# Kernel optimization log

Measured on AMD Instinct MI355X. Metric: run time of the kernel, lower is better.

Reference implementation:

```python
import jax, jax.numpy as jnp
import numpy as np

TAU = 0.1
HARD_K = 32
MIN_OVERLAP = 4
PAIR_WEIGHTS = [("view", "cart", 0.2), ("cart", "purchase", 1.0), ("view", "purchase", 1.0)]


def setup_inputs() -> dict:
    key = jax.random.key(0)
    ks = jax.random.split(key, 6)
    U, D = 100000, 128
    return {
        "emb_view": jax.random.normal(ks[0], (U, D), dtype=jnp.float32),
        "emb_cart": jax.random.normal(ks[1], (U, D), dtype=jnp.float32),
        "emb_purchase": jax.random.normal(ks[2], (U, D), dtype=jnp.float32),
        "users_view": jax.random.randint(ks[3], (20000,), 0, U, dtype=jnp.int64),
        "users_cart": jax.random.randint(ks[4], (15000,), 0, U, dtype=jnp.int64),
        "users_purchase": jax.random.randint(ks[5], (10000,), 0, U, dtype=jnp.int64),
    }


def _l2norm(x):
    # F.normalize(x, dim=-1): x / max(||x||, eps)
    n = jnp.linalg.norm(x, axis=-1, keepdims=True)
    return x / jnp.maximum(n, 1e-12)


def _directional(z_weak, z_strong, tau, hard_k):
    N = z_strong.shape[0]
    if N < 2:
        return jnp.zeros((), dtype=z_strong.dtype)
    z_w = _l2norm(jax.lax.stop_gradient(z_weak))  # weak side is detached
    z_s = _l2norm(z_strong)
    sim = (z_s @ z_w.T) / tau  # [N, N]
    pos = jnp.diagonal(sim)    # positive logits, labels = arange(N)
    n_hard = min(hard_k, N - 1)
    if 0 < n_hard < N - 1:
        neg_only = jnp.where(jnp.eye(N, dtype=bool), -jnp.inf, sim)
        hard_neg, _ = jax.lax.top_k(neg_only, n_hard)          # [N, n_hard]
        logits = jnp.concatenate([pos[:, None], hard_neg], 1)  # [N, 1+n_hard]
        return jnp.mean(jax.scipy.special.logsumexp(logits, axis=1) - pos)
    # full-softmax CE with label i for row i
    return jnp.mean(jax.scipy.special.logsumexp(sim, axis=1) - pos)


def reference(emb_view, emb_cart, emb_purchase, users_view, users_cart, users_purchase):
    embs = {"view": emb_view, "cart": emb_cart, "purchase": emb_purchase}
    users = {
        "view": np.asarray(users_view),
        "cart": np.asarray(users_cart),
        "purchase": np.asarray(users_purchase),
    }
    loss = jnp.zeros((), dtype=emb_view.dtype)
    for weak, strong, w in PAIR_WEIGHTS:
        u_w, u_s = users[weak], users[strong]
        if u_w.size == 0 or u_s.size == 0:
            continue
        # common_pair = u_w[isin(u_w, u_s)] : keeps u_w order and duplicates
        common = u_w[np.isin(u_w, u_s)]
        if common.size < MIN_OVERLAP:
            continue
        idx = jnp.asarray(common)
        loss = loss + w * _directional(embs[weak][idx], embs[strong][idx], TAU, HARD_K)
    return loss
```

## Files before the change

kernel.cpp:

```cpp
#include <hip/hip_runtime.h>
#include <hip/hip_bf16.h>
#include <math.h>

#define D 128
#define NEG_INF (-3.0e38f)
#define LDA 136

#define C0 3200
#define C1 1792
#define C2 2304
#define T0 25
#define T1 14
#define T2 18

typedef __attribute__((ext_vector_type(8))) short bf16x8;
typedef __attribute__((ext_vector_type(8))) unsigned short u16x8;
typedef __attribute__((ext_vector_type(4))) float f32x4;

__device__ __forceinline__ float wredf_add(float v) {
#pragma unroll
  for (int m = 32; m; m >>= 1) v += __shfl_xor(v, m, 64);
  return v;
}
__device__ __forceinline__ float wredf_max(float v) {
#pragma unroll
  for (int m = 32; m; m >>= 1) v = fmaxf(v, __shfl_xor(v, m, 64));
  return v;
}
__device__ __forceinline__ float wredf_min(float v) {
#pragma unroll
  for (int m = 32; m; m >>= 1) v = fminf(v, __shfl_xor(v, m, 64));
  return v;
}
__device__ __forceinline__ int wredi_add(int v) {
#pragma unroll
  for (int m = 32; m; m >>= 1) v += __shfl_xor(v, m, 64);
  return v;
}

__global__ void build_masks_k(const int* __restrict__ uc, int nc,
                              const int* __restrict__ up, int npu,
                              unsigned* __restrict__ mc, unsigned* __restrict__ mp) {
  int t = blockIdx.x * blockDim.x + threadIdx.x;
  if (t < nc) {
    int u = uc[t];
    atomicOr(&mc[u >> 5], 1u << (u & 31));
  } else {
    int t2 = t - nc;
    if (t2 < npu) {
      int u = up[t2];
      atomicOr(&mp[u >> 5], 1u << (u & 31));
    }
  }
}

__global__ void filter_k(const int* __restrict__ uv, int nv,
                         const int* __restrict__ uc, int nc,
                         const unsigned* __restrict__ mc, const unsigned* __restrict__ mp,
                         int* __restrict__ c0, int* __restrict__ c1, int* __restrict__ c2,
                         int* __restrict__ counts, int s1, int s2) {
  int t = blockIdx.x * blockDim.x + threadIdx.x;
  int lane = threadIdx.x & 63;
  const int* src;
  const unsigned* m;
  int* dst;
  int* cnt;
  int n, cap, base;
  if (t < s1) {
    src = uv; n = nv; m = mc; dst = c0; cnt = counts + 0; cap = C0; base = t;
  } else if (t < s2) {
    src = uc; n = nc; m = mp; dst = c1; cnt = counts + 1; cap = C1; base = t - s1;
  } else {
    src = uv; n = nv; m = mp; dst = c2; cnt = counts + 2; cap = C2; base = t - s2;
  }
  bool match = false;
  int u = 0;
  if (base < n) {
    u = src[base];
    match = (m[u >> 5] >> (u & 31)) & 1u;
  }
  unsigned long long b = __ballot(match);
  int tot = __popcll(b);
  int idx0 = 0;
  if (lane == 0 && tot) idx0 = atomicAdd(cnt, tot);
  idx0 = __shfl(idx0, 0, 64);
  if (match) {
    int p = idx0 + __popcll(b & ((1ull << lane) - 1));
    if (p < cap) dst[p] = u;
  }
}

struct GatherArgs {
  const float* emb[6];
  const int* com[6];
  const int* cnt[6];
  short* dst[6];
  int start[7];
};

__global__ __launch_bounds__(256) void gather_norm_k(GatherArgs ga) {
  int wid = threadIdx.x >> 6, lane = threadIdx.x & 63;
  int g = blockIdx.x * 4 + wid;
  if (g >= ga.start[6]) return;
  int s = 0;
#pragma unroll
  for (int t = 1; t < 6; ++t)
    if (g >= ga.start[t]) s = t;
  int r = g - ga.start[s];
  int cap = ga.start[s + 1] - ga.start[s];
  int N = min(*ga.cnt[s], cap);
  short* drow = ga.dst[s] + (size_t)r * D + lane * 2;
  if (r >= N) {
    *(ushort2*)drow = make_ushort2(0, 0);
    return;
  }
  int u = ga.com[s][r];
  const float* src = ga.emb[s] + (size_t)u * D;
  float2 v = *(const float2*)(src + lane * 2);
  float ss = v.x * v.x + v.y * v.y;
  ss = wredf_add(ss);
  float inv = 1.0f / fmaxf(sqrtf(ss), 1e-12f);
  __hip_bfloat16 h0 = __float2bfloat16(v.x * inv);
  __hip_bfloat16 h1 = __float2bfloat16(v.y * inv);
  ushort2 o;
  o.x = *(unsigned short*)&h0;
  o.y = *(unsigned short*)&h1;
  *(ushort2*)drow = o;
}

__device__ __forceinline__ void gemm_tile(const short* __restrict__ A, const short* __restrict__ B,
                                          unsigned short* __restrict__ C, int ldc, int bx, int by,
                                          short* As, short* Bs, int tid) {
  int rb = by * 128, cb = bx * 128;
  int rrow = tid >> 4, rcol = (tid & 15) * 8;
#pragma unroll
  for (int pass = 0; pass < 8; ++pass) {
    int row = pass * 16 + rrow;
    uint4 va = *(const uint4*)(A + (size_t)(rb + row) * D + rcol);
    uint4 vb = *(const uint4*)(B + (size_t)(cb + row) * D + rcol);
    *(uint4*)(&As[row * LDA + rcol]) = va;
    *(uint4*)(&Bs[row * LDA + rcol]) = vb;
  }
  __syncthreads();
  int wave = tid >> 6, lane = tid & 63;
  int wr = (wave >> 1) * 64, wc = (wave & 1) * 64;
  int ln = lane & 15, quad = lane >> 4;
  f32x4 acc[4][4] = {};
#pragma unroll
  for (int ks = 0; ks < 4; ++ks) {
    int ko = ks * 32 + quad * 8;
    bf16x8 af[4], bg[4];
#pragma unroll
    for (int i = 0; i < 4; ++i) af[i] = *(const bf16x8*)(&As[(wr + i * 16 + ln) * LDA + ko]);
#pragma unroll
    for (int j = 0; j < 4; ++j) bg[j] = *(const bf16x8*)(&Bs[(wc + j * 16 + ln) * LDA + ko]);
#pragma unroll
    for (int i = 0; i < 4; ++i)
#pragma unroll
      for (int j = 0; j < 4; ++j)
        acc[i][j] = __builtin_amdgcn_mfma_f32_16x16x32_bf16(af[i], bg[j], acc[i][j], 0, 0, 0);
  }
#pragma unroll
  for (int i = 0; i < 4; ++i)
#pragma unroll
    for (int j = 0; j < 4; ++j) {
      int col = cb + wc + j * 16 + ln;
#pragma unroll
      for (int r = 0; r < 4; ++r) {
        int row = rb + wr + i * 16 + quad * 4 + r;
        __hip_bfloat16 h = __float2bfloat16(acc[i][j][r] * 10.0f);
        C[(size_t)row * ldc + col] = *(unsigned short*)&h;
      }
    }
}

struct GemmAllArgs {
  const short *zs0, *zw0, *zs1, *zw1, *zs2, *zw2;
  unsigned short *s0, *s1, *s2;
};

__global__ __launch_bounds__(256) void gemm_all_k(GemmAllArgs ga) {
  __shared__ __align__(16) short As[128 * LDA];
  __shared__ __align__(16) short Bs[128 * LDA];
  int tid = threadIdx.x;
  int b = blockIdx.x;
  if (b < T0 * T0) {
    gemm_tile(ga.zs0, ga.zw0, ga.s0, C0, b % T0, b / T0, As, Bs, tid);
  } else if (b < T0 * T0 + T1 * T1) {
    int t = b - T0 * T0;
    gemm_tile(ga.zs1, ga.zw1, ga.s1, C1, t % T1, t / T1, As, Bs, tid);
  } else {
    int t = b - T0 * T0 - T1 * T1;
    gemm_tile(ga.zs2, ga.zw2, ga.s2, C2, t % T2, t / T2, As, Bs, tid);
  }
}

template <int NL>
__device__ __forceinline__ void select_rows(const unsigned short* __restrict__ sim, int ldc, int N,
                                            int i, int lane, double* __restrict__ slot) {
  const unsigned short* row = sim + (size_t)i * ldc;
  float vals[NL * 8];
  float posl = NEG_INF;
#pragma unroll
  for (int L = 0; L < NL; ++L) {
    int base = L * 512 + lane * 8;
    u16x8 raw = {0, 0, 0, 0, 0, 0, 0, 0};
    if (L * 512 < N) raw = *(const u16x8*)(row + base);
#pragma unroll
    for (int c = 0; c < 8; ++c) {
      int j = base + c;
      float v = __uint_as_float((unsigned)raw[c] << 16);
      if (j >= N) v = NEG_INF;
      if (j == i) { posl = v; v = NEG_INF; }
      vals[L * 8 + c] = v;
    }
  }
  float pos = __shfl(posl, (i & 511) >> 3, 64);
  float m = NEG_INF;
#pragma unroll
  for (int s = 0; s < NL * 8; ++s) m = fmaxf(m, vals[s]);
  m = wredf_max(m);
  int K = min(32, N - 1);
  float lo = -20.0f, hi = m + 1e-3f;
  for (int it = 0; it < 16; ++it) {
    float mid = 0.5f * (lo + hi);
    int c = 0;
#pragma unroll
    for (int s = 0; s < NL * 8; ++s) c += (vals[s] > mid) ? 1 : 0;
    c = wredi_add(c);
    if (c >= K) lo = mid; else hi = mid;
  }
  float M = fmaxf(m, pos);
  float sum = 0.0f, vmin = 3.0e38f;
  int cnt = 0;
#pragma unroll
  for (int s = 0; s < NL * 8; ++s) {
    float v = vals[s];
    bool in = v > lo;
    float e = __expf(v - M);
    if (in) { sum += e; cnt++; vmin = fminf(vmin, v); }
  }
  sum = wredf_add(sum);
  cnt = wredi_add(cnt);
  vmin = wredf_min(vmin);
  float corr = (cnt > K) ? (float)(cnt - K) * __expf(vmin - M) : 0.0f;
  float lse = M + __logf(sum - corr + __expf(pos - M));
  if (lane == 0) atomicAdd(slot, (double)(lse - pos));
}

__global__ __launch_bounds__(256) void select_all_k(const unsigned short* __restrict__ sim0,
                                                    const unsigned short* __restrict__ sim1,
                                                    const unsigned short* __restrict__ sim2,
                                                    const int* __restrict__ counts,
                                                    double* __restrict__ partials) {
  int wid = threadIdx.x >> 6, lane = threadIdx.x & 63;
  int b = blockIdx.x;
  if (b < C0 / 4) {
    int N = min(counts[0], C0);
    int i = b * 4 + wid;
    if (i < N) select_rows<7>(sim0, C0, N, i, lane, partials + 0 * 64 + (b & 63));
  } else if (b < C0 / 4 + C1 / 4) {
    int bb = b - C0 / 4;
    int N = min(counts[1], C1);
    int i = bb * 4 + wid;
    if (i < N) select_rows<4>(sim1, C1, N, i, lane, partials + 64 + (bb & 63));
  } else {
    int bb = b - C0 / 4 - C1 / 4;
    int N = min(counts[2], C2);
    int i = bb * 4 + wid;
    if (i < N) select_rows<5>(sim2, C2, N, i, lane, partials + 128 + (bb & 63));
  }
}

__global__ void finalize_k(const int* __restrict__ counts, const double* __restrict__ partials,
                           float* __restrict__ out, int ok) {
  if (threadIdx.x != 0 || blockIdx.x != 0) return;
  if (!ok) { out[0] = -12345.0f; return; }
  const float w[3] = {0.2f, 1.0f, 1.0f};
  const int caps[3] = {C0, C1, C2};
  float tot = 0.0f;
  for (int p = 0; p < 3; ++p) {
    double s = 0.0;
    for (int k = 0; k < 64; ++k) s += partials[p * 64 + k];
    int N = min(counts[p], caps[p]);
    if (N >= 4) tot += w[p] * (float)(s / (double)N);
  }
  out[0] = tot;
}

extern "C" void kernel_launch(void* const* d_in, const int* in_sizes, int n_in,
                              void* d_out, int out_size, void* d_ws, size_t ws_size,
                              hipStream_t stream) {
  const float* emb_view = (const float*)d_in[0];
  const float* emb_cart = (const float*)d_in[1];
  const float* emb_pur  = (const float*)d_in[2];
  const int* u_view = (const int*)d_in[3];
  const int* u_cart = (const int*)d_in[4];
  const int* u_pur  = (const int*)d_in[5];
  int nv = in_sizes[3], nc = in_sizes[4], np = in_sizes[5];
  int U = in_sizes[0] / D;

  size_t off = 2048;
  auto alloc = [&](size_t b) {
    size_t o = (off + 255) & ~(size_t)255;
    off = o + b;
    return o;
  };
  size_t maskWords = (size_t)(U + 31) / 32;
  size_t mask0_off = alloc(maskWords * 4);
  size_t mask1_off = alloc(maskWords * 4);
  size_t zero_end = off;
  size_t com0_off = alloc((size_t)C0 * 4);
  size_t com1_off = alloc((size_t)C1 * 4);
  size_t com2_off = alloc((size_t)C2 * 4);
  size_t zw0_off = alloc((size_t)C0 * D * 2);
  size_t zs0_off = alloc((size_t)C0 * D * 2);
  size_t zw1_off = alloc((size_t)C1 * D * 2);
  size_t zs1_off = alloc((size_t)C1 * D * 2);
  size_t zw2_off = alloc((size_t)C2 * D * 2);
  size_t zs2_off = alloc((size_t)C2 * D * 2);
  size_t sim0_off = alloc((size_t)C0 * C0 * 2);
  size_t sim1_off = alloc((size_t)C1 * C1 * 2);
  size_t sim2_off = alloc((size_t)C2 * C2 * 2);
  (void)alloc(1024);
  int ws_ok = (off <= ws_size) ? 1 : 0;

  char* ws = (char*)d_ws;
  int* counts = (int*)ws;
  double* partials = (double*)(ws + 256);
  unsigned* mask_c = (unsigned*)(ws + mask0_off);
  unsigned* mask_p = (unsigned*)(ws + mask1_off);
  int* com0 = (int*)(ws + com0_off);
  int* com1 = (int*)(ws + com1_off);
  int* com2 = (int*)(ws + com2_off);
  short* zw0 = (short*)(ws + zw0_off);
  short* zs0 = (short*)(ws + zs0_off);
  short* zw1 = (short*)(ws + zw1_off);
  short* zs1 = (short*)(ws + zs1_off);
  short* zw2 = (short*)(ws + zw2_off);
  short* zs2 = (short*)(ws + zs2_off);
  unsigned short* sim0 = (unsigned short*)(ws + sim0_off);
  unsigned short* sim1 = (unsigned short*)(ws + sim1_off);
  unsigned short* sim2 = (unsigned short*)(ws + sim2_off);

  if (ws_ok) {
    hipMemsetAsync(d_ws, 0, zero_end, stream);

    int t_masks = nc + np;
    build_masks_k<<<(t_masks + 255) / 256, 256, 0, stream>>>(u_cart, nc, u_pur, np, mask_c, mask_p);

    int s1 = ((nv + 255) / 256) * 256;
    int s2 = s1 + ((nc + 255) / 256) * 256;
    int t_filt = s2 + ((nv + 255) / 256) * 256;
    filter_k<<<t_filt / 256, 256, 0, stream>>>(u_view, nv, u_cart, nc, mask_c, mask_p,
                                               com0, com1, com2, counts, s1, s2);

    GatherArgs ga;
    const float* embs[6] = {emb_view, emb_cart, emb_cart, emb_pur, emb_view, emb_pur};
    const int* coms[6] = {com0, com0, com1, com1, com2, com2};
    const int* cnts[6] = {counts + 0, counts + 0, counts + 1, counts + 1, counts + 2, counts + 2};
    short* dsts[6] = {zw0, zs0, zw1, zs1, zw2, zs2};
    int caps6[6] = {C0, C0, C1, C1, C2, C2};
    int cum = 0;
    for (int s = 0; s < 6; ++s) {
      ga.emb[s] = embs[s];
      ga.com[s] = coms[s];
      ga.cnt[s] = cnts[s];
      ga.dst[s] = dsts[s];
      ga.start[s] = cum;
      cum += caps6[s];
    }
    ga.start[6] = cum;
    gather_norm_k<<<cum / 4, 256, 0, stream>>>(ga);

    GemmAllArgs gar;
    gar.zs0 = zs0; gar.zw0 = zw0; gar.s0 = sim0;
    gar.zs1 = zs1; gar.zw1 = zw1; gar.s1 = sim1;
    gar.zs2 = zs2; gar.zw2 = zw2; gar.s2 = sim2;
    gemm_all_k<<<T0 * T0 + T1 * T1 + T2 * T2, 256, 0, stream>>>(gar);

    select_all_k<<<C0 / 4 + C1 / 4 + C2 / 4, 256, 0, stream>>>(sim0, sim1, sim2, counts, partials);
  }

  finalize_k<<<1, 1, 0, stream>>>(counts, partials, (float*)d_out, ws_ok);
}
```

Measured before the change: 217.0 us.

## Fuse preprocessing and GEMM into a cooperative kernel; fold finalize into select

Zeroing, mask build, filter, gather-normalize and the similarity GEMM now run in one cooperative persistent kernel separated by grid syncs. A fallback launches the old-style separate kernels if the cooperative launch fails. The finalize step moves into the select kernel through a last-block-done atomic counter, and the gather uses float4 loads with half-wave rows. The top-k threshold search now counts with ballot/popcount instead of shuffle reductions and starts from a tighter lower bound. The aim is fewer kernel launches, less launch overhead and cheaper reductions, at the cost of grid-sync overhead and occupancy limits from the cooperative grid size.

```diff
diff --git a/kernel.cpp b/kernel.cpp
--- a/kernel.cpp
+++ b/kernel.cpp
@@ -1,6 +1,9 @@
 #include <hip/hip_runtime.h>
 #include <hip/hip_bf16.h>
+#include <hip/hip_cooperative_groups.h>
 #include <math.h>
+
+namespace cg = cooperative_groups;
 
 #define D 128
 #define NEG_INF (-3.0e38f)
@@ -12,6 +15,8 @@
 #define T0 25
 #define T1 14
 #define T2 18
+#define NTILES (T0 * T0 + T1 * T1 + T2 * T2)
+#define NSEL (C0 / 4 + C1 / 4 + C2 / 4)
 
 typedef __attribute__((ext_vector_type(8))) short bf16x8;
 typedef __attribute__((ext_vector_type(8))) unsigned short u16x8;
@@ -32,35 +37,32 @@
   for (int m = 32; m; m >>= 1) v = fminf(v, __shfl_xor(v, m, 64));
   return v;
 }
-__device__ __forceinline__ int wredi_add(int v) {
+__device__ __forceinline__ double wredd_add(double v) {
 #pragma unroll
   for (int m = 32; m; m >>= 1) v += __shfl_xor(v, m, 64);
   return v;
 }
 
-__global__ void build_masks_k(const int* __restrict__ uc, int nc,
-                              const int* __restrict__ up, int npu,
-                              unsigned* __restrict__ mc, unsigned* __restrict__ mp) {
-  int t = blockIdx.x * blockDim.x + threadIdx.x;
-  if (t < nc) {
-    int u = uc[t];
-    atomicOr(&mc[u >> 5], 1u << (u & 31));
-  } else {
-    int t2 = t - nc;
-    if (t2 < npu) {
-      int u = up[t2];
+__device__ __forceinline__ void phase_masks(const int* uc, int nc, const int* up, int np,
+                                            unsigned* mc, unsigned* mp, int gtid, int nthreads) {
+  int tot = nc + np;
+  for (int t = gtid; t < tot; t += nthreads) {
+    if (t < nc) {
+      int u = uc[t];
+      atomicOr(&mc[u >> 5], 1u << (u & 31));
+    } else {
+      int u = up[t - nc];
       atomicOr(&mp[u >> 5], 1u << (u & 31));
     }
   }
 }
 
-__global__ void filter_k(const int* __restrict__ uv, int nv,
-                         const int* __restrict__ uc, int nc,
-                         const unsigned* __restrict__ mc, const unsigned* __restrict__ mp,
-                         int* __restrict__ c0, int* __restrict__ c1, int* __restrict__ c2,
-                         int* __restrict__ counts, int s1, int s2) {
-  int t = blockIdx.x * blockDim.x + threadIdx.x;
-  int lane = threadIdx.x & 63;
+__device__ __forceinline__ void phase_filter(const int* uv, int nv, const int* uc, int nc,
+                                             const unsigned* mc, const unsigned* mp,
+                                             int* c0, int* c1, int* c2, int* counts,
+                                             int s1, int s2, int t_filt, int gtid, int lane) {
+  int t = gtid;
+  if (t >= t_filt) return;
   const int* src;
   const unsigned* m;
   int* dst;
@@ -90,42 +92,27 @@
   }
 }
 
-struct GatherArgs {
-  const float* emb[6];
-  const int* com[6];
-  const int* cnt[6];
-  short* dst[6];
-  int start[7];
-};
-
-__global__ __launch_bounds__(256) void gather_norm_k(GatherArgs ga) {
-  int wid = threadIdx.x >> 6, lane = threadIdx.x & 63;
-  int g = blockIdx.x * 4 + wid;
-  if (g >= ga.start[6]) return;
-  int s = 0;
-#pragma unroll
-  for (int t = 1; t < 6; ++t)
-    if (g >= ga.start[t]) s = t;
-  int r = g - ga.start[s];
-  int cap = ga.start[s + 1] - ga.start[s];
-  int N = min(*ga.cnt[s], cap);
-  short* drow = ga.dst[s] + (size_t)r * D + lane * 2;
-  if (r >= N) {
-    *(ushort2*)drow = make_ushort2(0, 0);
-    return;
-  }
-  int u = ga.com[s][r];
-  const float* src = ga.emb[s] + (size_t)u * D;
-  float2 v = *(const float2*)(src + lane * 2);
-  float ss = v.x * v.x + v.y * v.y;
-  ss = wredf_add(ss);
-  float inv = 1.0f / fmaxf(sqrtf(ss), 1e-12f);
-  __hip_bfloat16 h0 = __float2bfloat16(v.x * inv);
-  __hip_bfloat16 h1 = __float2bfloat16(v.y * inv);
-  ushort2 o;
-  o.x = *(unsigned short*)&h0;
-  o.y = *(unsigned short*)&h1;
-  *(ushort2*)drow = o;
+__device__ __forceinline__ void gather_seg(const float* __restrict__ emb, const int* __restrict__ com,
+                                           const int* __restrict__ cntp, short* __restrict__ dst,
+                                           int cap, int hw, int nhw, int l) {
+  for (int r = hw; r < cap; r += nhw) {
+    int N = min(*cntp, cap);
+    short* drow = dst + (size_t)r * D + l * 4;
+    if (r >= N) {
+      *(ushort4*)drow = make_ushort4(0, 0, 0, 0);
+      continue;
+    }
+    int u = com[r];
+    float4 v = *(const float4*)(emb + (size_t)u * D + l * 4);
+    float ss = v.x * v.x + v.y * v.y + v.z * v.z + v.w * v.w;
+#pragma unroll
+    for (int m = 16; m; m >>= 1) ss += __shfl_xor(ss, m, 64);
+    float inv = 1.0f / fmaxf(sqrtf(ss), 1e-12f);
+    __hip_bfloat16 h0 = __float2bfloat16(v.x * inv), h1 = __float2bfloat16(v.y * inv);
+    __hip_bfloat16 h2 = __float2bfloat16(v.z * inv), h3 = __float2bfloat16(v.w * inv);
+    *(ushort4*)drow = make_ushort4(*(unsigned short*)&h0, *(unsigned short*)&h1,
+                                   *(unsigned short*)&h2, *(unsigned short*)&h3);
+  }
 }
 
 __device__ __forceinline__ void gemm_tile(const short* __restrict__ A, const short* __restrict__ B,
@@ -172,27 +159,96 @@
         C[(size_t)row * ldc + col] = *(unsigned short*)&h;
       }
     }
-}
-
-struct GemmAllArgs {
-  const short *zs0, *zw0, *zs1, *zw1, *zs2, *zw2;
-  unsigned short *s0, *s1, *s2;
+  __syncthreads();
+}
+
+__device__ __forceinline__ void gemm_dispatch(int t, const short* zs0, const short* zw0,
+                                              const short* zs1, const short* zw1,
+                                              const short* zs2, const short* zw2,
+                                              unsigned short* s0, unsigned short* s1,
+                                              unsigned short* s2, short* As, short* Bs, int tid) {
+  if (t < T0 * T0) {
+    gemm_tile(zs0, zw0, s0, C0, t % T0, t / T0, As, Bs, tid);
+  } else if (t < T0 * T0 + T1 * T1) {
+    int u = t - T0 * T0;
+    gemm_tile(zs1, zw1, s1, C1, u % T1, u / T1, As, Bs, tid);
+  } else {
+    int u = t - T0 * T0 - T1 * T1;
+    gemm_tile(zs2, zw2, s2, C2, u % T2, u / T2, As, Bs, tid);
+  }
+}
+
+struct CoopArgs {
+  const int *uv, *uc, *up;
+  int nv, nc, np, s1, s2, t_filt;
+  unsigned* zero_base;
+  int zeroWords;
+  unsigned *mc, *mp;
+  int* counts;
+  int *c0, *c1, *c2;
+  const float *ev, *ec, *ep;
+  short *zw0, *zs0, *zw1, *zs1, *zw2, *zs2;
+  unsigned short *s0, *s1p, *s2p;
 };
 
-__global__ __launch_bounds__(256) void gemm_all_k(GemmAllArgs ga) {
+__global__ __launch_bounds__(256, 2) void coop_all_k(CoopArgs a) {
   __shared__ __align__(16) short As[128 * LDA];
   __shared__ __align__(16) short Bs[128 * LDA];
+  cg::grid_group grid = cg::this_grid();
   int tid = threadIdx.x;
-  int b = blockIdx.x;
-  if (b < T0 * T0) {
-    gemm_tile(ga.zs0, ga.zw0, ga.s0, C0, b % T0, b / T0, As, Bs, tid);
-  } else if (b < T0 * T0 + T1 * T1) {
-    int t = b - T0 * T0;
-    gemm_tile(ga.zs1, ga.zw1, ga.s1, C1, t % T1, t / T1, As, Bs, tid);
-  } else {
-    int t = b - T0 * T0 - T1 * T1;
-    gemm_tile(ga.zs2, ga.zw2, ga.s2, C2, t % T2, t / T2, As, Bs, tid);
-  }
+  int gtid = blockIdx.x * 256 + tid;
+  int nthreads = gridDim.x * 256;
+  int lane = tid & 63;
+
+  for (int w = gtid; w < a.zeroWords; w += nthreads) a.zero_base[w] = 0u;
+  grid.sync();
+  phase_masks(a.uc, a.nc, a.up, a.np, a.mc, a.mp, gtid, nthreads);
+  grid.sync();
+  phase_filter(a.uv, a.nv, a.uc, a.nc, a.mc, a.mp, a.c0, a.c1, a.c2, a.counts,
+               a.s1, a.s2, a.t_filt, gtid, lane);
+  grid.sync();
+  {
+    int hw = gtid >> 5, nhw = nthreads >> 5, l = tid & 31;
+    gather_seg(a.ev, a.c0, a.counts + 0, a.zw0, C0, hw, nhw, l);
+    gather_seg(a.ec, a.c0, a.counts + 0, a.zs0, C0, hw, nhw, l);
+    gather_seg(a.ec, a.c1, a.counts + 1, a.zw1, C1, hw, nhw, l);
+    gather_seg(a.ep, a.c1, a.counts + 1, a.zs1, C1, hw, nhw, l);
+    gather_seg(a.ev, a.c2, a.counts + 2, a.zw2, C2, hw, nhw, l);
+    gather_seg(a.ep, a.c2, a.counts + 2, a.zs2, C2, hw, nhw, l);
+  }
+  grid.sync();
+  for (int t = blockIdx.x; t < NTILES; t += gridDim.x)
+    gemm_dispatch(t, a.zs0, a.zw0, a.zs1, a.zw1, a.zs2, a.zw2, a.s0, a.s1p, a.s2p, As, Bs, tid);
+}
+
+__global__ void zero_k(unsigned* base, int words) {
+  int t = blockIdx.x * blockDim.x + threadIdx.x;
+  for (int w = t; w < words; w += gridDim.x * blockDim.x) base[w] = 0u;
+}
+__global__ void masks_k(const int* uc, int nc, const int* up, int np, unsigned* mc, unsigned* mp) {
+  phase_masks(uc, nc, up, np, mc, mp, blockIdx.x * blockDim.x + threadIdx.x, gridDim.x * blockDim.x);
+}
+__global__ void filter_only_k(const int* uv, int nv, const int* uc, int nc,
+                              const unsigned* mc, const unsigned* mp,
+                              int* c0, int* c1, int* c2, int* counts, int s1, int s2, int t_filt) {
+  phase_filter(uv, nv, uc, nc, mc, mp, c0, c1, c2, counts, s1, s2, t_filt,
+               blockIdx.x * blockDim.x + threadIdx.x, threadIdx.x & 63);
+}
+__global__ __launch_bounds__(256) void gather_k(CoopArgs a) {
+  int gtid = blockIdx.x * 256 + threadIdx.x;
+  int hw = gtid >> 5, nhw = (gridDim.x * 256) >> 5, l = threadIdx.x & 31;
+  gather_seg(a.ev, a.c0, a.counts + 0, a.zw0, C0, hw, nhw, l);
+  gather_seg(a.ec, a.c0, a.counts + 0, a.zs0, C0, hw, nhw, l);
+  gather_seg(a.ec, a.c1, a.counts + 1, a.zw1, C1, hw, nhw, l);
+  gather_seg(a.ep, a.c1, a.counts + 1, a.zs1, C1, hw, nhw, l);
+  gather_seg(a.ev, a.c2, a.counts + 2, a.zw2, C2, hw, nhw, l);
+  gather_seg(a.ep, a.c2, a.counts + 2, a.zs2, C2, hw, nhw, l);
+}
+__global__ __launch_bounds__(256) void gemm_only_k(CoopArgs a) {
+  __shared__ __align__(16) short As[128 * LDA];
+  __shared__ __align__(16) short Bs[128 * LDA];
+  gemm_dispatch(blockIdx.x, a.zs0, a.zw0, a.zs1, a.zw1, a.zs2, a.zw2, a.s0, a.s1p, a.s2p,
+                As, Bs, threadIdx.x);
 }
 
 template <int NL>
@@ -221,13 +277,12 @@
   for (int s = 0; s < NL * 8; ++s) m = fmaxf(m, vals[s]);
   m = wredf_max(m);
   int K = min(32, N - 1);
-  float lo = -20.0f, hi = m + 1e-3f;
+  float lo = -10.2f, hi = m + 1e-3f;
   for (int it = 0; it < 16; ++it) {
     float mid = 0.5f * (lo + hi);
     int c = 0;
 #pragma unroll
-    for (int s = 0; s < NL * 8; ++s) c += (vals[s] > mid) ? 1 : 0;
-    c = wredi_add(c);
+    for (int s = 0; s < NL * 8; ++s) c += __popcll(__ballot(vals[s] > mid));
     if (c >= K) lo = mid; else hi = mid;
   }
   float M = fmaxf(m, pos);
@@ -236,23 +291,33 @@
 #pragma unroll
   for (int s = 0; s < NL * 8; ++s) {
     float v = vals[s];
-    bool in = v > lo;
-    float e = __expf(v - M);
-    if (in) { sum += e; cnt++; vmin = fminf(vmin, v); }
+    if (v > lo) {
+      sum += __expf(v - M);
+      cnt++;
+      vmin = fminf(vmin, v);
+    }
   }
   sum = wredf_add(sum);
-  cnt = wredi_add(cnt);
+  cnt = (int)__popcll(__ballot(true)) == 64 ? cnt : cnt;
+  {
+    int ctot = 0;
+#pragma unroll
+    for (int s = 0; s < NL * 8; ++s) ctot += __popcll(__ballot(vals[s] > lo));
+    cnt = ctot;
+  }
   vmin = wredf_min(vmin);
   float corr = (cnt > K) ? (float)(cnt - K) * __expf(vmin - M) : 0.0f;
   float lse = M + __logf(sum - corr + __expf(pos - M));
   if (lane == 0) atomicAdd(slot, (double)(lse - pos));
 }
 
-__global__ __launch_bounds__(256) void select_all_k(const unsigned short* __restrict__ sim0,
+__global__ __launch_bounds__(256) void select_fin_k(const unsigned short* __restrict__ sim0,
                                                     const unsigned short* __restrict__ sim1,
                                                     const unsigned short* __restrict__ sim2,
                                                     const int* __restrict__ counts,
-                                                    double* __restrict__ partials) {
+                                                    double* __restrict__ partials,
+                                                    unsigned* __restrict__ done,
+                                                    float* __restrict__ out) {
   int wid = threadIdx.x >> 6, lane = threadIdx.x & 63;
   int b = blockIdx.x;
   if (b < C0 / 4) {
@@ -270,22 +335,35 @@
     int i = bb * 4 + wid;
     if (i < N) select_rows<5>(sim2, C2, N, i, lane, partials + 128 + (bb & 63));
   }
-}
-
-__global__ void finalize_k(const int* __restrict__ counts, const double* __restrict__ partials,
-                           float* __restrict__ out, int ok) {
-  if (threadIdx.x != 0 || blockIdx.x != 0) return;
-  if (!ok) { out[0] = -12345.0f; return; }
-  const float w[3] = {0.2f, 1.0f, 1.0f};
-  const int caps[3] = {C0, C1, C2};
-  float tot = 0.0f;
-  for (int p = 0; p < 3; ++p) {
-    double s = 0.0;
-    for (int k = 0; k < 64; ++k) s += partials[p * 64 + k];
-    int N = min(counts[p], caps[p]);
-    if (N >= 4) tot += w[p] * (float)(s / (double)N);
-  }
-  out[0] = tot;
+  __shared__ int lastf;
+  __shared__ double ps[4];
+  __syncthreads();
+  if (threadIdx.x == 0) {
+    __threadfence();
+    unsigned old = atomicAdd(done, 1u);
+    lastf = (old == (unsigned)(gridDim.x - 1)) ? 1 : 0;
+  }
+  __syncthreads();
+  if (!lastf) return;
+  double v = 0.0;
+  if (threadIdx.x < 192) v = atomicAdd(&partials[threadIdx.x], 0.0);
+  v = wredd_add(v);
+  if (lane == 0 && wid < 3) ps[wid] = v;
+  __syncthreads();
+  if (threadIdx.x == 0) {
+    const float w[3] = {0.2f, 1.0f, 1.0f};
+    const int caps[3] = {C0, C1, C2};
+    float tot = 0.0f;
+    for (int p = 0; p < 3; ++p) {
+      int N = min(counts[p], caps[p]);
+      if (N >= 4) tot += w[p] * (float)(ps[p] / (double)N);
+    }
+    out[0] = tot;
+  }
+}
+
+__global__ void sentinel_k(float* out) {
+  if (threadIdx.x == 0 && blockIdx.x == 0) out[0] = -12345.0f;
 }
 
 extern "C" void kernel_launch(void* const* d_in, const int* in_sizes, int n_in,
@@ -300,15 +378,16 @@
   int nv = in_sizes[3], nc = in_sizes[4], np = in_sizes[5];
   int U = in_sizes[0] / D;
 
-  size_t off = 2048;
+  size_t off = 64;
   auto alloc = [&](size_t b) {
     size_t o = (off + 255) & ~(size_t)255;
     off = o + b;
     return o;
   };
-  size_t maskWords = (size_t)(U + 31) / 32;
-  size_t mask0_off = alloc(maskWords * 4);
-  size_t mask1_off = alloc(maskWords * 4);
+  size_t partials_off = alloc(192 * 8);
+  size_t maskBytes = ((size_t)(U + 31) / 32) * 4;
+  size_t mask0_off = alloc(maskBytes);
+  size_t mask1_off = alloc(maskBytes);
   size_t zero_end = off;
   size_t com0_off = alloc((size_t)C0 * 4);
   size_t com1_off = alloc((size_t)C1 * 4);
@@ -326,61 +405,50 @@
   int ws_ok = (off <= ws_size) ? 1 : 0;
 
   char* ws = (char*)d_ws;
-  int* counts = (int*)ws;
-  double* partials = (double*)(ws + 256);
-  unsigned* mask_c = (unsigned*)(ws + mask0_off);
-  unsigned* mask_p = (unsigned*)(ws + mask1_off);
-  int* com0 = (int*)(ws + com0_off);
-  int* com1 = (int*)(ws + com1_off);
-  int* com2 = (int*)(ws + com2_off);
-  short* zw0 = (short*)(ws + zw0_off);
-  short* zs0 = (short*)(ws + zs0_off);
-  short* zw1 = (short*)(ws + zw1_off);
-  short* zs1 = (short*)(ws + zs1_off);
-  short* zw2 = (short*)(ws + zw2_off);
-  short* zs2 = (short*)(ws + zs2_off);
-  unsigned short* sim0 = (unsigned short*)(ws + sim0_off);
-  unsigned short* sim1 = (unsigned short*)(ws + sim1_off);
-  unsigned short* sim2 = (unsigned short*)(ws + sim2_off);
-
-  if (ws_ok) {
-    hipMemsetAsync(d_ws, 0, zero_end, stream);
-
-    int t_masks = nc + np;
-    build_masks_k<<<(t_masks + 255) / 256, 256, 0, stream>>>(u_cart, nc, u_pur, np, mask_c, mask_p);
-
-    int s1 = ((nv + 255) / 256) * 256;
-    int s2 = s1 + ((nc + 255) / 256) * 256;
-    int t_filt = s2 + ((nv + 255) / 256) * 256;
-    filter_k<<<t_filt / 256, 256, 0, stream>>>(u_view, nv, u_cart, nc, mask_c, mask_p,
-                                               com0, com1, com2, counts, s1, s2);
-
-    GatherArgs ga;
-    const float* embs[6] = {emb_view, emb_cart, emb_cart, emb_pur, emb_view, emb_pur};
-    const int* coms[6] = {com0, com0, com1, com1, com2, com2};
-    const int* cnts[6] = {counts + 0, counts + 0, counts + 1, counts + 1, counts + 2, counts + 2};
-    short* dsts[6] = {zw0, zs0, zw1, zs1, zw2, zs2};
-    int caps6[6] = {C0, C0, C1, C1, C2, C2};
-    int cum = 0;
-    for (int s = 0; s < 6; ++s) {
-      ga.emb[s] = embs[s];
-      ga.com[s] = coms[s];
-      ga.cnt[s] = cnts[s];
-      ga.dst[s] = dsts[s];
-      ga.start[s] = cum;
-      cum += caps6[s];
-    }
-    ga.start[6] = cum;
-    gather_norm_k<<<cum / 4, 256, 0, stream>>>(ga);
-
-    GemmAllArgs gar;
-    gar.zs0 = zs0; gar.zw0 = zw0; gar.s0 = sim0;
-    gar.zs1 = zs1; gar.zw1 = zw1; gar.s1 = sim1;
-    gar.zs2 = zs2; gar.zw2 = zw2; gar.s2 = sim2;
-    gemm_all_k<<<T0 * T0 + T1 * T1 + T2 * T2, 256, 0, stream>>>(gar);
-
-    select_all_k<<<C0 / 4 + C1 / 4 + C2 / 4, 256, 0, stream>>>(sim0, sim1, sim2, counts, partials);
-  }
-
-  finalize_k<<<1, 1, 0, stream>>>(counts, partials, (float*)d_out, ws_ok);
-}
+  if (!ws_ok) {
+    sentinel_k<<<1, 1, 0, stream>>>((float*)d_out);
+    return;
+  }
+
+  CoopArgs a;
+  a.uv = u_view; a.uc = u_cart; a.up = u_pur;
+  a.nv = nv; a.nc = nc; a.np = np;
+  a.s1 = ((nv + 255) / 256) * 256;
+  a.s2 = a.s1 + ((nc + 255) / 256) * 256;
+  a.t_filt = a.s2 + ((nv + 255) / 256) * 256;
+  a.zero_base = (unsigned*)ws;
+  a.zeroWords = (int)((zero_end + 3) / 4);
+  a.mc = (unsigned*)(ws + mask0_off);
+  a.mp = (unsigned*)(ws + mask1_off);
+  a.counts = (int*)ws;
+  a.c0 = (int*)(ws + com0_off);
+  a.c1 = (int*)(ws + com1_off);
+  a.c2 = (int*)(ws + com2_off);
+  a.ev = emb_view; a.ec = emb_cart; a.ep = emb_pur;
+  a.zw0 = (short*)(ws + zw0_off); a.zs0 = (short*)(ws + zs0_off);
+  a.zw1 = (short*)(ws + zw1_off); a.zs1 = (short*)(ws + zs1_off);
+  a.zw2 = (short*)(ws + zw2_off); a.zs2 = (short*)(ws + zs2_off);
+  a.s0 = (unsigned short*)(ws + sim0_off);
+  a.s1p = (unsigned short*)(ws + sim1_off);
+  a.s2p = (unsigned short*)(ws + sim2_off);
+
+  double* partials = (double*)(ws + partials_off);
+  unsigned* done = (unsigned*)(ws + 12);
+
+  void* kp[] = {(void*)&a};
+  hipError_t e = hipLaunchCooperativeKernel((const void*)coop_all_k, dim3(512), dim3(256),
+                                            kp, 0, stream);
+  if (e != hipSuccess) {
+    (void)hipGetLastError();
+    zero_k<<<64, 256, 0, stream>>>(a.zero_base, a.zeroWords);
+    masks_k<<<(nc + np + 255) / 256, 256, 0, stream>>>(u_cart, nc, u_pur, np, a.mc, a.mp);
+    filter_only_k<<<a.t_filt / 256, 256, 0, stream>>>(u_view, nv, u_cart, nc, a.mc, a.mp,
+                                                      a.c0, a.c1, a.c2, a.counts,
+                                                      a.s1, a.s2, a.t_filt);
+    gather_k<<<512, 256, 0, stream>>>(a);
+    gemm_only_k<<<NTILES, 256, 0, stream>>>(a);
+  }
+
+  select_fin_k<<<NSEL, 256, 0, stream>>>(a.s0, a.s1p, a.s2p, a.counts, partials, done,
+                                         (float*)d_out);
+}
```

Result: slower. 435.2 us (+100.5%).
